# Performance work log

Hardware: AMD Instinct MI355X
Metric: run time of the kernel (lower is better)

The kernel has to match this reference:

```python
import jax, jax.numpy as jnp
import numpy as np

N_HEADS = 16
KEY_DIM = 64
D_MODEL = 1024
B, NQ, NK = 2, 2048, 2048


def setup_inputs() -> dict:
    key = jax.random.key(0)
    ks = jax.random.split(key, 12)
    s = 0.02
    return {
        "Q": jax.random.normal(ks[0], (B, NQ, D_MODEL), jnp.float32),
        "V": jax.random.normal(ks[1], (B, NK, D_MODEL), jnp.float32),
        "K": jax.random.normal(ks[2], (B, NK, D_MODEL), jnp.float32),
        "mask": jax.random.randint(ks[3], (B, NQ, NK), 0, 2).astype(jnp.float32),
        "Wq": jax.random.normal(ks[4], (D_MODEL, N_HEADS * KEY_DIM), jnp.float32) * s,
        "bq_": jnp.zeros((N_HEADS * KEY_DIM,), jnp.float32),
        "Wk": jax.random.normal(ks[5], (D_MODEL, N_HEADS * KEY_DIM), jnp.float32) * s,
        "bk_": jnp.zeros((N_HEADS * KEY_DIM,), jnp.float32),
        "Wv": jax.random.normal(ks[6], (D_MODEL, N_HEADS * KEY_DIM), jnp.float32) * s,
        "bv_": jnp.zeros((N_HEADS * KEY_DIM,), jnp.float32),
        "Wo": jax.random.normal(ks[7], (N_HEADS * KEY_DIM, D_MODEL), jnp.float32) * s,
        "bo_": jnp.zeros((D_MODEL,), jnp.float32),
    }


def _split_heads(x, b, n, h, d):
    # [b, n, h*d] -> [h*b, n, d]  (head-major flatten, as in the TF code)
    return x.reshape(b, n, h, d).transpose(2, 0, 1, 3).reshape(h * b, n, d)


def reference(Q, V, K, mask, Wq, bq_, Wk, bk_, Wv, bv_, Wo, bo_):
    b, nq, _ = Q.shape
    nk = K.shape[1]
    h, dk = N_HEADS, KEY_DIM
    Qd = _split_heads(Q @ Wq + bq_, b, nq, h, dk)
    Kd = _split_heads(K @ Wk + bk_, b, nk, h, dk)
    Vd = _split_heads(V @ Wv + bv_, b, nk, h, dk)
    # scores [h*b, nq, nk]
    U = jnp.einsum('bnd,bmd->bnm', Qd, Kd) / jnp.sqrt(jnp.float32(dk))
    # faithful quirk: mask repeated batch-major while heads are head-major
    mask_rep = jnp.repeat(mask, h, axis=0)  # [b*h, nq, nk]
    U = U * mask_rep
    A = jax.nn.softmax(U, axis=-1)
    out = jnp.einsum('bnm,bmd->bnd', A, Vd)  # [h*b, nq, dk]
    out = out.reshape(h, b, nq, dk).transpose(1, 2, 0, 3).reshape(b, nq, h * dk)
    return out @ Wo + bo_
```

## Files before the change

### kernel.cpp

```cpp
#include <hip/hip_runtime.h>
#include <hip/hip_bf16.h>
#include <stdint.h>

#define NHEADS 16
#define DKEY   64
#define DMODEL 1024
#define BATCH  2
#define SEQ    2048

using bf16x8 = __bf16 __attribute__((ext_vector_type(8)));
using bf16x4 = __bf16 __attribute__((ext_vector_type(4)));
using f32x4  = float __attribute__((ext_vector_type(4)));

__device__ __forceinline__ void gl_lds16(const void* g, void* l) {
  __builtin_amdgcn_global_load_lds(
      (__attribute__((address_space(1))) void*)(uintptr_t)g,
      (__attribute__((address_space(3))) void*)(uint32_t)(uintptr_t)l,
      16, 0, 0);
}

__global__ __launch_bounds__(256) void wtrans_kernel(
    const float* __restrict__ Wo, const float* __restrict__ Wq,
    const float* __restrict__ Wk, const float* __restrict__ Wv,
    __bf16* __restrict__ WTbase)
{
  const float* W = (blockIdx.z == 0) ? Wo : (blockIdx.z == 1) ? Wq
                   : (blockIdx.z == 2) ? Wk : Wv;
  __bf16* WT = WTbase + (size_t)blockIdx.z * DMODEL * DMODEL;
  __shared__ float tile[64][65];
  const int tid = threadIdx.x;
  const int k0 = blockIdx.x * 64, n0 = blockIdx.y * 64;
  const int cx = tid & 63, ry = tid >> 6;
#pragma unroll
  for (int i = 0; i < 16; ++i) {
    int kl = i * 4 + ry;
    tile[cx][kl] = W[(size_t)(k0 + kl) * DMODEL + n0 + cx];
  }
  __syncthreads();
#pragma unroll
  for (int i = 0; i < 16; ++i) {
    int nl = i * 4 + ry;
    WT[(size_t)(n0 + nl) * DMODEL + k0 + cx] = (__bf16)tile[nl][cx];
  }
}

__global__ __launch_bounds__(256) void maskpack_kernel(
    const float* __restrict__ mask, unsigned long long* __restrict__ bits)
{
  const int gtid = blockIdx.x * 256 + threadIdx.x;
  const int w    = gtid >> 6;
  const int lane = threadIdx.x & 63;
  float v = mask[(size_t)w * 64 + lane];
  unsigned long long m = __ballot(v != 0.0f);
  if (lane == 0) bits[w] = m;
}

__global__ __launch_bounds__(256, 4) void qkv_gemm_kernel(
    const float* __restrict__ Qf, const float* __restrict__ Kf, const float* __restrict__ Vf,
    const __bf16* __restrict__ WT,
    const float* __restrict__ bq, const float* __restrict__ bk, const float* __restrict__ bv,
    __bf16* __restrict__ Qd, __bf16* __restrict__ Kd, __bf16* __restrict__ Vt)
{
  __shared__ __bf16 sA[128 * 32];
  __shared__ __bf16 sB[128 * 32];
  const int z = blockIdx.z;
  const float* A     = (z == 0) ? Qf : (z == 1) ? Kf : Vf;
  const __bf16* BT   = WT + (size_t)(z + 1) * DMODEL * DMODEL;
  const float*  bias = (z == 0) ? bq : (z == 1) ? bk : bv;

  const int tid  = threadIdx.x;
  const int lane = tid & 63;
  const int g    = lane >> 4, l15 = lane & 15;
  const int wid  = tid >> 6;
  const int wr   = wid >> 1, wc = wid & 1;
  const int m0   = blockIdx.x * 128, n0 = blockIdx.y * 128;

  const int srow  = tid >> 2;
  const int sslot = tid & 3;

  f32x4 acc[4][4] = {};

  for (int ks = 0; ks < 32; ++ks) {
    const int k0 = ks * 32;
    f32x4 a0[2], a1[2];
#pragma unroll
    for (int c2 = 0; c2 < 2; ++c2) {
      const float* p = A + (size_t)(m0 + c2 * 64 + srow) * DMODEL + k0 + sslot * 8;
      a0[c2] = *(const f32x4*)p;
      a1[c2] = *(const f32x4*)(p + 4);
    }
#pragma unroll
    for (int c2 = 0; c2 < 2; ++c2) {
      char* lb = (char*)sB + c2 * 4096 + wid * 1024;
      gl_lds16(BT + (size_t)(n0 + c2 * 64 + srow) * DMODEL + k0 + sslot * 8, lb);
    }
#pragma unroll
    for (int c2 = 0; c2 < 2; ++c2) {
      bf16x8 v;
#pragma unroll
      for (int j = 0; j < 4; ++j) { v[j] = (__bf16)a0[c2][j]; v[j + 4] = (__bf16)a1[c2][j]; }
      *(bf16x8*)((char*)sA + (c2 * 64 + srow) * 64 + sslot * 16) = v;
    }
    asm volatile("s_waitcnt vmcnt(0)" ::: "memory");
    __syncthreads();

    bf16x8 af[4], bfr[4];
#pragma unroll
    for (int mt = 0; mt < 4; ++mt)
      af[mt] = *(const bf16x8*)((const char*)sA + (wr * 64 + mt * 16 + l15) * 64 + g * 16);
#pragma unroll
    for (int nt = 0; nt < 4; ++nt)
      bfr[nt] = *(const bf16x8*)((const char*)sB + (wc * 64 + nt * 16 + l15) * 64 + g * 16);
#pragma unroll
    for (int mt = 0; mt < 4; ++mt)
#pragma unroll
      for (int nt = 0; nt < 4; ++nt)
        acc[mt][nt] = __builtin_amdgcn_mfma_f32_16x16x32_bf16(af[mt], bfr[nt], acc[mt][nt], 0, 0, 0);
    __syncthreads();
  }

#pragma unroll
  for (int nt = 0; nt < 4; ++nt) {
    const int gn = n0 + wc * 64 + nt * 16 + l15;
    const float bvv = bias[gn];
    const int h = gn >> 6, d = gn & 63;
#pragma unroll
    for (int mt = 0; mt < 4; ++mt) {
      const int gmb = m0 + wr * 64 + mt * 16 + g * 4;
      const int b = gmb >> 11, nr = gmb & 2047;
      if (z == 2) {
        bf16x4 pk;
#pragma unroll
        for (int r = 0; r < 4; ++r) pk[r] = (__bf16)(acc[mt][nt][r] + bvv);
        *(bf16x4*)(Vt + ((size_t)(h * 2 + b) * DKEY + d) * SEQ + nr) = pk;
      } else {
        __bf16* outp = z ? Kd : Qd;
#pragma unroll
        for (int r = 0; r < 4; ++r)
          outp[((size_t)(h * 2 + b) * SEQ + nr + r) * DKEY + d] = (__bf16)(acc[mt][nt][r] + bvv);
      }
    }
  }
}

__global__ __launch_bounds__(256, 4) void out_gemm_kernel(
    const __bf16* __restrict__ AO, const __bf16* __restrict__ WTo,
    const float* __restrict__ bo, float* __restrict__ out)
{
  __shared__ __bf16 sA[128 * 32];
  __shared__ __bf16 sB[64 * 32];
  const int tid  = threadIdx.x;
  const int lane = tid & 63;
  const int g    = lane >> 4, l15 = lane & 15;
  const int wid  = tid >> 6;
  const int wr   = wid >> 1, wc = wid & 1;
  const int m0   = blockIdx.x * 128, n0 = blockIdx.y * 64;

  const int srow  = tid >> 2;
  const int sslot = tid & 3;

  f32x4 acc[4][2] = {};

  for (int ks = 0; ks < 32; ++ks) {
    const int k0 = ks * 32;
#pragma unroll
    for (int c2 = 0; c2 < 2; ++c2) {
      char* la = (char*)sA + c2 * 4096 + wid * 1024;
      gl_lds16(AO + (size_t)(m0 + c2 * 64 + srow) * DMODEL + k0 + sslot * 8, la);
    }
    {
      char* lb = (char*)sB + wid * 1024;
      gl_lds16(WTo + (size_t)(n0 + srow) * DMODEL + k0 + sslot * 8, lb);
    }
    asm volatile("s_waitcnt vmcnt(0)" ::: "memory");
    __syncthreads();

    bf16x8 af[4], bfr[2];
#pragma unroll
    for (int mt = 0; mt < 4; ++mt)
      af[mt] = *(const bf16x8*)((const char*)sA + (wr * 64 + mt * 16 + l15) * 64 + g * 16);
#pragma unroll
    for (int nt = 0; nt < 2; ++nt)
      bfr[nt] = *(const bf16x8*)((const char*)sB + (wc * 32 + nt * 16 + l15) * 64 + g * 16);
#pragma unroll
    for (int mt = 0; mt < 4; ++mt)
#pragma unroll
      for (int nt = 0; nt < 2; ++nt)
        acc[mt][nt] = __builtin_amdgcn_mfma_f32_16x16x32_bf16(af[mt], bfr[nt], acc[mt][nt], 0, 0, 0);
    __syncthreads();
  }

#pragma unroll
  for (int nt = 0; nt < 2; ++nt) {
    const int gn = n0 + wc * 32 + nt * 16 + l15;
    const float bvv = bo[gn];
#pragma unroll
    for (int mt = 0; mt < 4; ++mt) {
      const int gmb = m0 + wr * 64 + mt * 16 + g * 4;
#pragma unroll
      for (int r = 0; r < 4; ++r)
        out[(size_t)(gmb + r) * DMODEL + gn] = acc[mt][nt][r] + bvv;
    }
  }
}

__global__ __launch_bounds__(256, 4) void attn_kernel(
    const __bf16* __restrict__ Qd, const __bf16* __restrict__ Kd,
    const __bf16* __restrict__ Vt, const unsigned long long* __restrict__ mbits,
    __bf16* __restrict__ AO)
{
  __shared__ __bf16 sK[64 * 64];
  __shared__ __bf16 sV[64 * 64];
  __shared__ __bf16 sP[4][16 * 64];

  const int tid = threadIdx.x, lane = tid & 63, wid = tid >> 6;
  const int g = lane >> 4, c = lane & 15;
  const int q0 = blockIdx.x * 64;
  const int hb = blockIdx.y;
  const int h = hb >> 1, b = hb & 1;
  const int bp = hb >> 4;

  const __bf16* Qbase = Qd + (size_t)hb * SEQ * DKEY;
  const __bf16* Kbase = Kd + (size_t)hb * SEQ * DKEY;
  const __bf16* Vbase = Vt + (size_t)hb * DKEY * SEQ;

  const int qr = q0 + wid * 16 + c;
  bf16x8 aq[2];
  aq[0] = *(const bf16x8*)(Qbase + (size_t)qr * DKEY + g * 8);
  aq[1] = *(const bf16x8*)(Qbase + (size_t)qr * DKEY + 32 + g * 8);

  f32x4 o[4] = {};
  float rs[4] = {0.f, 0.f, 0.f, 0.f};

  for (int kv0 = 0; kv0 < SEQ; kv0 += 64) {
#pragma unroll
    for (int c2 = 0; c2 < 2; ++c2) {
      const int ch = c2 * 256 + tid;
      const int row = ch >> 3, sl = ch & 7;
      char* lk = (char*)sK + c2 * 4096 + wid * 1024;
      char* lv = (char*)sV + c2 * 4096 + wid * 1024;
      gl_lds16(Kbase + (size_t)(kv0 + row) * DKEY + ((sl ^ (row & 7)) * 8), lk);
      gl_lds16(Vbase + (size_t)row * SEQ + kv0 + ((sl ^ (row & 7)) * 8), lv);
    }
    asm volatile("s_waitcnt vmcnt(0)" ::: "memory");
    __syncthreads();

    unsigned long long mw[4];
#pragma unroll
    for (int r = 0; r < 4; ++r) {
      int q = q0 + wid * 16 + g * 4 + r;
      mw[r] = mbits[((size_t)bp * SEQ + q) * 32 + (kv0 >> 6)];
    }

#pragma unroll
    for (int t = 0; t < 4; ++t) {
      f32x4 u = {0.f, 0.f, 0.f, 0.f};
#pragma unroll
      for (int kk = 0; kk < 2; ++kk) {
        int row = t * 16 + c;
        bf16x8 kf = *(const bf16x8*)((char*)sK + row * 128 + (((g + kk * 4) ^ (row & 7)) * 16));
        u = __builtin_amdgcn_mfma_f32_16x16x32_bf16(aq[kk], kf, u, 0, 0, 0);
      }
#pragma unroll
      for (int r = 0; r < 4; ++r) {
        int col = t * 16 + c;
        float s = u[r] * 0.125f;
        s = ((mw[r] >> col) & 1ULL) ? s : 0.0f;
        float p = __expf(s);
        rs[r] += p;
        int qrl = g * 4 + r;
        int sp = (col >> 3) ^ (qrl & 7);
        *(__bf16*)((char*)&sP[wid][0] + qrl * 128 + sp * 16 + (col & 7) * 2) = (__bf16)p;
      }
    }
    asm volatile("s_waitcnt lgkmcnt(0)" ::: "memory");

    bf16x8 ap[2];
#pragma unroll
    for (int kk = 0; kk < 2; ++kk) {
      int sp = (kk * 4 + g) ^ (c & 7);
      ap[kk] = *(const bf16x8*)((char*)&sP[wid][0] + c * 128 + sp * 16);
    }
    __builtin_amdgcn_s_setprio(1);
#pragma unroll
    for (int dt = 0; dt < 4; ++dt) {
#pragma unroll
      for (int kk = 0; kk < 2; ++kk) {
        int row = dt * 16 + c;
        bf16x8 vf = *(const bf16x8*)((char*)sV + row * 128 + (((kk * 4 + g) ^ (row & 7)) * 16));
        o[dt] = __builtin_amdgcn_mfma_f32_16x16x32_bf16(ap[kk], vf, o[dt], 0, 0, 0);
      }
    }
    __builtin_amdgcn_s_setprio(0);
    __syncthreads();
  }

#pragma unroll
  for (int r = 0; r < 4; ++r) {
    float v = rs[r];
    v += __shfl_xor(v, 1, 16);
    v += __shfl_xor(v, 2, 16);
    v += __shfl_xor(v, 4, 16);
    v += __shfl_xor(v, 8, 16);
    rs[r] = v;
  }

#pragma unroll
  for (int dt = 0; dt < 4; ++dt) {
#pragma unroll
    for (int r = 0; r < 4; ++r) {
      int q = q0 + wid * 16 + g * 4 + r;
      int dk = dt * 16 + c;
      AO[((size_t)b * SEQ + q) * DMODEL + h * 64 + dk] = (__bf16)(o[dt][r] / rs[r]);
    }
  }
}

extern "C" void kernel_launch(void* const* d_in, const int* in_sizes, int n_in,
                              void* d_out, int out_size, void* d_ws, size_t ws_size,
                              hipStream_t stream)
{
  (void)in_sizes; (void)n_in; (void)out_size; (void)ws_size;
  const float* Q    = (const float*)d_in[0];
  const float* V    = (const float*)d_in[1];
  const float* K    = (const float*)d_in[2];
  const float* mask = (const float*)d_in[3];
  const float* Wq   = (const float*)d_in[4];
  const float* bq   = (const float*)d_in[5];
  const float* Wk   = (const float*)d_in[6];
  const float* bk   = (const float*)d_in[7];
  const float* Wv   = (const float*)d_in[8];
  const float* bv   = (const float*)d_in[9];
  const float* Wo   = (const float*)d_in[10];
  const float* bo   = (const float*)d_in[11];
  float* out = (float*)d_out;

  char* ws = (char*)d_ws;
  const size_t MB = 1024 * 1024;
  __bf16* WT = (__bf16*)(ws);
  __bf16* AO = (__bf16*)(ws + 8 * MB);
  __bf16* Qd = (__bf16*)(ws + 16 * MB);
  __bf16* Kd = (__bf16*)(ws + 24 * MB);
  __bf16* Vt = (__bf16*)(ws + 32 * MB);
  unsigned long long* mbits = (unsigned long long*)(ws + 40 * MB);

  wtrans_kernel<<<dim3(16, 16, 4), 256, 0, stream>>>(Wo, Wq, Wk, Wv, WT);
  maskpack_kernel<<<dim3(32768), 256, 0, stream>>>(mask, mbits);
  qkv_gemm_kernel<<<dim3(32, 8, 3), 256, 0, stream>>>(Q, K, V, WT, bq, bk, bv, Qd, Kd, Vt);
  attn_kernel<<<dim3(32, 32), 256, 0, stream>>>(Qd, Kd, Vt, mbits, AO);
  out_gemm_kernel<<<dim3(32, 16), 256, 0, stream>>>(AO, WT, bo, out);
}
```

Baseline: 290.8 us.

## Double GEMM K-tile to 64 with XOR-swizzled LDS and fold softmax scale into Q

The QKV and output projection GEMMs now use a K-step of 64 instead of 32, which halves the loop iterations and barriers. The LDS tiles are XOR-swizzled to avoid bank conflicts on the wider rows, and QKV occupancy is lowered to 3 blocks per SM. The attention kernel no longer multiplies scores by 1/sqrt(dk) and calls __expf. Instead Q is pre-scaled by log2(e)/8 in the projection epilogue and exp2f is used, so per-score multiplies are removed. Rounding the pre-scaled Q to bf16 changes precision slightly.

```diff
diff --git a/kernel.cpp b/kernel.cpp
--- a/kernel.cpp
+++ b/kernel.cpp
@@ -1,12 +1,14 @@
 #include <hip/hip_runtime.h>
 #include <hip/hip_bf16.h>
 #include <stdint.h>
+#include <math.h>
 
 #define NHEADS 16
 #define DKEY   64
 #define DMODEL 1024
 #define BATCH  2
 #define SEQ    2048
+#define QSCALE 0.18033688011112042f
 
 using bf16x8 = __bf16 __attribute__((ext_vector_type(8)));
 using bf16x4 = __bf16 __attribute__((ext_vector_type(4)));
@@ -55,14 +57,14 @@
   if (lane == 0) bits[w] = m;
 }
 
-__global__ __launch_bounds__(256, 4) void qkv_gemm_kernel(
+__global__ __launch_bounds__(256, 3) void qkv_gemm_kernel(
     const float* __restrict__ Qf, const float* __restrict__ Kf, const float* __restrict__ Vf,
     const __bf16* __restrict__ WT,
     const float* __restrict__ bq, const float* __restrict__ bk, const float* __restrict__ bv,
     __bf16* __restrict__ Qd, __bf16* __restrict__ Kd, __bf16* __restrict__ Vt)
 {
-  __shared__ __bf16 sA[128 * 32];
-  __shared__ __bf16 sB[128 * 32];
+  __shared__ __bf16 sA[128 * 64];
+  __shared__ __bf16 sB[128 * 64];
   const int z = blockIdx.z;
   const float* A     = (z == 0) ? Qf : (z == 1) ? Kf : Vf;
   const __bf16* BT   = WT + (size_t)(z + 1) * DMODEL * DMODEL;
@@ -75,47 +77,57 @@
   const int wr   = wid >> 1, wc = wid & 1;
   const int m0   = blockIdx.x * 128, n0 = blockIdx.y * 128;
 
-  const int srow  = tid >> 2;
-  const int sslot = tid & 3;
+  const int srow8 = tid >> 3;
+  const int ssl8  = tid & 7;
 
   f32x4 acc[4][4] = {};
 
-  for (int ks = 0; ks < 32; ++ks) {
-    const int k0 = ks * 32;
-    f32x4 a0[2], a1[2];
-#pragma unroll
-    for (int c2 = 0; c2 < 2; ++c2) {
-      const float* p = A + (size_t)(m0 + c2 * 64 + srow) * DMODEL + k0 + sslot * 8;
-      a0[c2] = *(const f32x4*)p;
-      a1[c2] = *(const f32x4*)(p + 4);
-    }
-#pragma unroll
-    for (int c2 = 0; c2 < 2; ++c2) {
-      char* lb = (char*)sB + c2 * 4096 + wid * 1024;
-      gl_lds16(BT + (size_t)(n0 + c2 * 64 + srow) * DMODEL + k0 + sslot * 8, lb);
-    }
-#pragma unroll
-    for (int c2 = 0; c2 < 2; ++c2) {
+  for (int ks = 0; ks < 16; ++ks) {
+    const int k0 = ks * 64;
+    f32x4 a0[4], a1[4];
+#pragma unroll
+    for (int c4 = 0; c4 < 4; ++c4) {
+      const int row = c4 * 32 + srow8;
+      const float* p = A + (size_t)(m0 + row) * DMODEL + k0 + ssl8 * 8;
+      a0[c4] = *(const f32x4*)p;
+      a1[c4] = *(const f32x4*)(p + 4);
+    }
+#pragma unroll
+    for (int c4 = 0; c4 < 4; ++c4) {
+      const int row = c4 * 32 + srow8;
+      char* lb = (char*)sB + c4 * 4096 + wid * 1024;
+      gl_lds16(BT + (size_t)(n0 + row) * DMODEL + k0 + ((ssl8 ^ (row & 7)) * 8), lb);
+    }
+#pragma unroll
+    for (int c4 = 0; c4 < 4; ++c4) {
+      const int row = c4 * 32 + srow8;
       bf16x8 v;
 #pragma unroll
-      for (int j = 0; j < 4; ++j) { v[j] = (__bf16)a0[c2][j]; v[j + 4] = (__bf16)a1[c2][j]; }
-      *(bf16x8*)((char*)sA + (c2 * 64 + srow) * 64 + sslot * 16) = v;
+      for (int j = 0; j < 4; ++j) { v[j] = (__bf16)a0[c4][j]; v[j + 4] = (__bf16)a1[c4][j]; }
+      *(bf16x8*)((char*)sA + row * 128 + ((ssl8 ^ (row & 7)) * 16)) = v;
     }
     asm volatile("s_waitcnt vmcnt(0)" ::: "memory");
     __syncthreads();
 
-    bf16x8 af[4], bfr[4];
-#pragma unroll
-    for (int mt = 0; mt < 4; ++mt)
-      af[mt] = *(const bf16x8*)((const char*)sA + (wr * 64 + mt * 16 + l15) * 64 + g * 16);
-#pragma unroll
-    for (int nt = 0; nt < 4; ++nt)
-      bfr[nt] = *(const bf16x8*)((const char*)sB + (wc * 64 + nt * 16 + l15) * 64 + g * 16);
-#pragma unroll
-    for (int mt = 0; mt < 4; ++mt)
-#pragma unroll
-      for (int nt = 0; nt < 4; ++nt)
-        acc[mt][nt] = __builtin_amdgcn_mfma_f32_16x16x32_bf16(af[mt], bfr[nt], acc[mt][nt], 0, 0, 0);
+#pragma unroll
+    for (int kk = 0; kk < 2; ++kk) {
+      bf16x8 af[4], bfr[4];
+#pragma unroll
+      for (int mt = 0; mt < 4; ++mt) {
+        const int row = wr * 64 + mt * 16 + l15;
+        af[mt] = *(const bf16x8*)((const char*)sA + row * 128 + (((kk * 4 + g) ^ (row & 7)) * 16));
+      }
+#pragma unroll
+      for (int nt = 0; nt < 4; ++nt) {
+        const int row = wc * 64 + nt * 16 + l15;
+        bfr[nt] = *(const bf16x8*)((const char*)sB + row * 128 + (((kk * 4 + g) ^ (row & 7)) * 16));
+      }
+#pragma unroll
+      for (int mt = 0; mt < 4; ++mt)
+#pragma unroll
+        for (int nt = 0; nt < 4; ++nt)
+          acc[mt][nt] = __builtin_amdgcn_mfma_f32_16x16x32_bf16(af[mt], bfr[nt], acc[mt][nt], 0, 0, 0);
+    }
     __syncthreads();
   }
 
@@ -133,11 +145,14 @@
 #pragma unroll
         for (int r = 0; r < 4; ++r) pk[r] = (__bf16)(acc[mt][nt][r] + bvv);
         *(bf16x4*)(Vt + ((size_t)(h * 2 + b) * DKEY + d) * SEQ + nr) = pk;
+      } else if (z == 0) {
+#pragma unroll
+        for (int r = 0; r < 4; ++r)
+          Qd[((size_t)(h * 2 + b) * SEQ + nr + r) * DKEY + d] = (__bf16)((acc[mt][nt][r] + bvv) * QSCALE);
       } else {
-        __bf16* outp = z ? Kd : Qd;
 #pragma unroll
         for (int r = 0; r < 4; ++r)
-          outp[((size_t)(h * 2 + b) * SEQ + nr + r) * DKEY + d] = (__bf16)(acc[mt][nt][r] + bvv);
+          Kd[((size_t)(h * 2 + b) * SEQ + nr + r) * DKEY + d] = (__bf16)(acc[mt][nt][r] + bvv);
       }
     }
   }
@@ -147,8 +162,8 @@
     const __bf16* __restrict__ AO, const __bf16* __restrict__ WTo,
     const float* __restrict__ bo, float* __restrict__ out)
 {
-  __shared__ __bf16 sA[128 * 32];
-  __shared__ __bf16 sB[64 * 32];
+  __shared__ __bf16 sA[128 * 64];
+  __shared__ __bf16 sB[64 * 64];
   const int tid  = threadIdx.x;
   const int lane = tid & 63;
   const int g    = lane >> 4, l15 = lane & 15;
@@ -156,37 +171,47 @@
   const int wr   = wid >> 1, wc = wid & 1;
   const int m0   = blockIdx.x * 128, n0 = blockIdx.y * 64;
 
-  const int srow  = tid >> 2;
-  const int sslot = tid & 3;
+  const int srow8 = tid >> 3;
+  const int ssl8  = tid & 7;
 
   f32x4 acc[4][2] = {};
 
-  for (int ks = 0; ks < 32; ++ks) {
-    const int k0 = ks * 32;
+  for (int ks = 0; ks < 16; ++ks) {
+    const int k0 = ks * 64;
+#pragma unroll
+    for (int c4 = 0; c4 < 4; ++c4) {
+      const int row = c4 * 32 + srow8;
+      char* la = (char*)sA + c4 * 4096 + wid * 1024;
+      gl_lds16(AO + (size_t)(m0 + row) * DMODEL + k0 + ((ssl8 ^ (row & 7)) * 8), la);
+    }
 #pragma unroll
     for (int c2 = 0; c2 < 2; ++c2) {
-      char* la = (char*)sA + c2 * 4096 + wid * 1024;
-      gl_lds16(AO + (size_t)(m0 + c2 * 64 + srow) * DMODEL + k0 + sslot * 8, la);
-    }
-    {
-      char* lb = (char*)sB + wid * 1024;
-      gl_lds16(WTo + (size_t)(n0 + srow) * DMODEL + k0 + sslot * 8, lb);
+      const int row = c2 * 32 + srow8;
+      char* lb = (char*)sB + c2 * 4096 + wid * 1024;
+      gl_lds16(WTo + (size_t)(n0 + row) * DMODEL + k0 + ((ssl8 ^ (row & 7)) * 8), lb);
     }
     asm volatile("s_waitcnt vmcnt(0)" ::: "memory");
     __syncthreads();
 
-    bf16x8 af[4], bfr[2];
-#pragma unroll
-    for (int mt = 0; mt < 4; ++mt)
-      af[mt] = *(const bf16x8*)((const char*)sA + (wr * 64 + mt * 16 + l15) * 64 + g * 16);
-#pragma unroll
-    for (int nt = 0; nt < 2; ++nt)
-      bfr[nt] = *(const bf16x8*)((const char*)sB + (wc * 32 + nt * 16 + l15) * 64 + g * 16);
-#pragma unroll
-    for (int mt = 0; mt < 4; ++mt)
-#pragma unroll
-      for (int nt = 0; nt < 2; ++nt)
-        acc[mt][nt] = __builtin_amdgcn_mfma_f32_16x16x32_bf16(af[mt], bfr[nt], acc[mt][nt], 0, 0, 0);
+#pragma unroll
+    for (int kk = 0; kk < 2; ++kk) {
+      bf16x8 af[4], bfr[2];
+#pragma unroll
+      for (int mt = 0; mt < 4; ++mt) {
+        const int row = wr * 64 + mt * 16 + l15;
+        af[mt] = *(const bf16x8*)((const char*)sA + row * 128 + (((kk * 4 + g) ^ (row & 7)) * 16));
+      }
+#pragma unroll
+      for (int nt = 0; nt < 2; ++nt) {
+        const int row = wc * 32 + nt * 16 + l15;
+        bfr[nt] = *(const bf16x8*)((const char*)sB + row * 128 + (((kk * 4 + g) ^ (row & 7)) * 16));
+      }
+#pragma unroll
+      for (int mt = 0; mt < 4; ++mt)
+#pragma unroll
+        for (int nt = 0; nt < 2; ++nt)
+          acc[mt][nt] = __builtin_amdgcn_mfma_f32_16x16x32_bf16(af[mt], bfr[nt], acc[mt][nt], 0, 0, 0);
+    }
     __syncthreads();
   }
 
@@ -264,9 +289,8 @@
 #pragma unroll
       for (int r = 0; r < 4; ++r) {
         int col = t * 16 + c;
-        float s = u[r] * 0.125f;
-        s = ((mw[r] >> col) & 1ULL) ? s : 0.0f;
-        float p = __expf(s);
+        float s = ((mw[r] >> col) & 1ULL) ? u[r] : 0.0f;
+        float p = exp2f(s);
         rs[r] += p;
         int qrl = g * 4 + r;
         int sp = (col >> 3) ^ (qrl & 7);
```

After: 281.5 us. 1.03x faster.
